# Performance work log

Measured on AMD Instinct MI355X. Metric: run time of the kernel, lower is better.

The kernel has to match this reference:

```python
import jax, jax.numpy as jnp
import numpy as np

K = 16  # FLAGS.num_neighbors
N = 2562  # ellipsoid vertices
B = 4     # FLAGS.batch_size
M = 16384 # points per cloud
D = 3     # coordinate dim


def _mean_neighborhood(coord, pc, k):
    # coord: [N, D] query vertices; pc: [B, D, M] point cloud (channels-first)
    x2 = jnp.sum(coord * coord, axis=1)[None, :, None]          # [1, N, 1]
    y2 = jnp.sum(pc * pc, axis=1)[:, None, :]                   # [B, 1, M]
    xy = jnp.einsum('nd,bdm->bnm', coord, pc)                   # [B, N, M]
    d2 = x2 + y2 - 2.0 * xy                                     # [B, N, M]
    _, idx = jax.lax.top_k(-d2, k)                               # [B, N, K] indices into M
    Y = jnp.transpose(pc, (0, 2, 1))                             # [B, M, D]
    bv = jnp.arange(pc.shape[0])[:, None, None]                  # [B, 1, 1]
    knnY = Y[bv, idx]                                            # [B, N, K, D]
    knnY_mean = jnp.mean(knnY, axis=2)                           # [B, N, D]
    return knnY_mean[0]                                          # [N, D] (matches knnY_mean[0])


def setup_inputs() -> dict:
    key = jax.random.key(0)
    ks = jax.random.split(key, 5)
    inputs = jax.random.normal(ks[0], (N, D), dtype=jnp.float32)
    pcs = [jax.random.normal(ks[i + 1], (B, D, M), dtype=jnp.float32) for i in range(4)]
    return {"inputs": inputs, "pc0": pcs[0], "pc1": pcs[1], "pc2": pcs[2], "pc3": pcs[3]}


def reference(inputs, pc0, pc1, pc2, pc3):
    s0 = _mean_neighborhood(inputs, pc0, K)
    s1 = _mean_neighborhood(inputs, pc1, K)
    s2 = _mean_neighborhood(inputs, pc2, K)
    s3 = _mean_neighborhood(inputs, pc3, K)
    return jnp.concatenate([inputs, s0, s1, s2, s3], axis=1)  # [N, 5*D]
```

## Files before the change

### kernel.cpp

```cpp
#include <hip/hip_runtime.h>
#include <stdint.h>
#include <math.h>

#define NQ    2562
#define MPTS  16384
#define QPB   4
#define NBQ   641
#define NT    (MPTS / 256)
#define CAP   320

__global__ __launch_bounds__(256)
void passthrough_kernel(const float* __restrict__ inp, float* __restrict__ out) {
    int gid = blockIdx.x * 256 + threadIdx.x;
    if (gid < NQ * 3) {
        int n = gid / 3, c = gid - n * 3;
        out[n * 15 + c] = inp[gid];
    }
}

__device__ __forceinline__ float sqsum3(float y0, float y1, float y2) {
    return __fadd_rn(__fadd_rn(__fmul_rn(y0, y0), __fmul_rn(y1, y1)),
                     __fmul_rn(y2, y2));
}
__device__ __forceinline__ float keyf(float xs, float a2, float b2, float c2,
                                      float y0, float y1, float y2, float ysq) {
    float u = fmaf(c2, y2, fmaf(b2, y1, __fmul_rn(a2, y0)));
    return __fsub_rn(__fadd_rn(xs, ysq), u);
}
__device__ __forceinline__ unsigned long long packkey(float k, int m) {
    uint32_t kb = __float_as_uint(k);
    kb ^= (uint32_t)((int32_t)kb >> 31) | 0x80000000u;
    return ((unsigned long long)kb << 32) | (unsigned)m;
}
__device__ __forceinline__ float unmapkey(unsigned long long pk) {
    uint32_t kb = (uint32_t)(pk >> 32);
    return __uint_as_float((kb & 0x80000000u) ? (kb ^ 0x80000000u) : ~kb);
}
__device__ __forceinline__ int prefix_lt(unsigned long long m) {
    return __builtin_amdgcn_mbcnt_hi((unsigned)(m >> 32),
           __builtin_amdgcn_mbcnt_lo((unsigned)m, 0u));
}

__device__ __forceinline__ unsigned long long sort64(unsigned long long v, int lane) {
#pragma unroll
    for (int k = 2; k <= 64; k <<= 1) {
#pragma unroll
        for (int j = k >> 1; j > 0; j >>= 1) {
            unsigned long long p = __shfl_xor(v, j);
            bool up = ((lane & k) == 0) == ((lane & j) == 0);
            bool sw = up ? (p < v) : (v < p);
            v = sw ? p : v;
        }
    }
    return v;
}

__device__ __forceinline__ float rebuild_q(unsigned long long* t16p,
                                           unsigned long long* S, int& cnt,
                                           int lane, bool fin) {
    int c = cnt;
    int full = c >> 6, rem = c & 63;
    int rounds = full + ((fin && rem) ? 1 : 0);
    unsigned long long v = ~0ULL;
    for (int rd = 0; rd < rounds; ++rd) {
        int i = (rd << 6) + lane;
        unsigned long long pk = (i < c) ? S[i] : ~0ULL;
        pk = sort64(pk, lane);
        unsigned long long bsw = __shfl(pk, (31 - lane) & 63);
        v = (lane < 16) ? t16p[lane & 15] : (lane < 32) ? bsw : ~0ULL;
#pragma unroll
        for (int j = 16; j > 0; j >>= 1) {
            unsigned long long p2 = __shfl_xor(v, j);
            bool keepmin = (lane & j) == 0;
            bool less = p2 < v;
            v = (keepmin == less) ? p2 : v;
        }
        if (lane < 16) t16p[lane] = v;
    }
    if (!fin) {
        if (lane < rem) S[lane] = S[(full << 6) + lane];
        cnt = rem;
    } else {
        cnt = 0;
    }
    return unmapkey(__shfl(v, 15));
}

__global__ __launch_bounds__(256)
void ysq_kernel(const float* __restrict__ pc0, const float* __restrict__ pc1,
                const float* __restrict__ pc2, const float* __restrict__ pc3,
                float* __restrict__ ysq) {
    int gid = blockIdx.x * 256 + threadIdx.x;
    int pc = gid >> 14, m = gid & (MPTS - 1);
    const float* P = (pc == 0) ? pc0 : (pc == 1) ? pc1 : (pc == 2) ? pc2 : pc3;
    ysq[gid] = sqsum3(P[m], P[MPTS + m], P[2 * MPTS + m]);
}

template <bool USE_YSQ>
__global__ __launch_bounds__(256)
void knn_kernel(const float* __restrict__ inp,
                const float* __restrict__ pc0, const float* __restrict__ pc1,
                const float* __restrict__ pc2, const float* __restrict__ pc3,
                const float* __restrict__ ysq,
                float* __restrict__ out) {
    const int b    = blockIdx.x;
    const int wid  = threadIdx.x >> 6;
    const int lane = threadIdx.x & 63;

    const int pc = b / NBQ;
    const int nb = b - pc * NBQ;
    const float* __restrict__ P = (pc == 0) ? pc0 : (pc == 1) ? pc1
                                : (pc == 2) ? pc2 : pc3;

    __shared__ float              tiles[2][4][256];
    __shared__ unsigned long long stk_sh[4][CAP];
    __shared__ unsigned long long t16_sh[4][16];

    if (lane < 16) t16_sh[wid][lane] = ~0ULL;

    float A2, B2, C2, XS;
    {
        int n = QPB * nb + wid;
        n = (n < NQ) ? n : (NQ - 1);
        float x0 = inp[n * 3 + 0];
        float x1 = inp[n * 3 + 1];
        float x2 = inp[n * 3 + 2];
        A2 = 2.0f * x0;
        B2 = 2.0f * x1;
        C2 = 2.0f * x2;
        XS = sqsum3(x0, x1, x2);
    }
    float tau;
    int   cnt = 0;

    const float* __restrict__ gch =
        (wid == 0) ? P : (wid == 1) ? (P + MPTS) : (wid == 2) ? (P + 2 * MPTS)
                   : (USE_YSQ ? (ysq + pc * MPTS) : P);

    auto push_tile = [&](int mofs, float k0, float k1, float k2, float k3) {
        unsigned long long b0 = __ballot(k0 <= tau);
        unsigned long long b1 = __ballot(k1 <= tau);
        unsigned long long b2 = __ballot(k2 <= tau);
        unsigned long long b3 = __ballot(k3 <= tau);
        int pre = prefix_lt(b0) + prefix_lt(b1) + prefix_lt(b2) + prefix_lt(b3);
        int tot = __popcll(b0) + __popcll(b1) + __popcll(b2) + __popcll(b3);
        int pos = cnt + pre;
        unsigned long long* S = stk_sh[wid];
        if (k0 <= tau) S[pos++] = packkey(k0, mofs + 0);
        if (k1 <= tau) S[pos++] = packkey(k1, mofs + 1);
        if (k2 <= tau) S[pos++] = packkey(k2, mofs + 2);
        if (k3 <= tau) S[pos++] = packkey(k3, mofs + 3);
        cnt += tot;
        if (cnt >= 64)
            tau = rebuild_q(t16_sh[wid], S, cnt, lane, false);
    };

    auto stage_load = [&](int t) -> float4 {
        if (USE_YSQ || wid < 3) {
            return *(const float4*)(gch + (t << 8) + (lane << 2));
        } else {
            const float* px = P + (t << 8) + (lane << 2);
            float4 a = *(const float4*)(px);
            float4 bq = *(const float4*)(px + MPTS);
            float4 cq = *(const float4*)(px + 2 * MPTS);
            float4 r;
            r.x = sqsum3(a.x, bq.x, cq.x);
            r.y = sqsum3(a.y, bq.y, cq.y);
            r.z = sqsum3(a.z, bq.z, cq.z);
            r.w = sqsum3(a.w, bq.w, cq.w);
            return r;
        }
    };

    {
        float4 s0 = stage_load(0);
        *(float4*)&tiles[0][wid][lane << 2] = s0;
    }
    __syncthreads();

    for (int t = 0; t < NT; ++t) {
        const int cur = t & 1;
        float4 stg;
        if (t + 1 < NT) stg = stage_load(t + 1);

        float4 xv = *(const float4*)&tiles[cur][0][lane << 2];
        float4 yv = *(const float4*)&tiles[cur][1][lane << 2];
        float4 zv = *(const float4*)&tiles[cur][2][lane << 2];
        float4 qv = *(const float4*)&tiles[cur][3][lane << 2];

        const int mofs = (t << 8) + (lane << 2);
        float k0 = keyf(XS, A2, B2, C2, xv.x, yv.x, zv.x, qv.x);
        float k1 = keyf(XS, A2, B2, C2, xv.y, yv.y, zv.y, qv.y);
        float k2 = keyf(XS, A2, B2, C2, xv.z, yv.z, zv.z, qv.z);
        float k3 = keyf(XS, A2, B2, C2, xv.w, yv.w, zv.w, qv.w);
        float km = fminf(fminf(k0, k1), fminf(k2, k3));

        if (t == 0) {
            float g = km;
            g = fminf(g, __shfl_xor(g, 1));
            g = fminf(g, __shfl_xor(g, 2));
            float m = g;
            m = fmaxf(m, __shfl_xor(m, 4));
            m = fmaxf(m, __shfl_xor(m, 8));
            m = fmaxf(m, __shfl_xor(m, 16));
            m = fmaxf(m, __shfl_xor(m, 32));
            tau = m;
            push_tile(mofs, k0, k1, k2, k3);
        } else if (__ballot(km <= tau)) {
            push_tile(mofs, k0, k1, k2, k3);
        }

        if (t + 1 < NT) *(float4*)&tiles[cur ^ 1][wid][lane << 2] = stg;

        __syncthreads();
    }

    if (cnt > 0)
        rebuild_q(t16_sh[wid], stk_sh[wid], cnt, lane, true);

    if (lane < 16) {
        unsigned long long v = t16_sh[wid][lane];
        int idx = (int)(unsigned)v;
        float gx = P[idx];
        float gy = P[MPTS + idx];
        float gz = P[2 * MPTS + idx];
#pragma unroll
        for (int off = 8; off > 0; off >>= 1) {
            gx += __shfl_down(gx, off, 16);
            gy += __shfl_down(gy, off, 16);
            gz += __shfl_down(gz, off, 16);
        }
        if (lane == 0) {
            int n = QPB * nb + wid;
            n = (n < NQ) ? n : (NQ - 1);
            float* o = out + n * 15 + 3 + 3 * pc;
            o[0] = gx * 0.0625f;
            o[1] = gy * 0.0625f;
            o[2] = gz * 0.0625f;
        }
    }
}

extern "C" void kernel_launch(void* const* d_in, const int* in_sizes, int n_in,
                              void* d_out, int out_size, void* d_ws, size_t ws_size,
                              hipStream_t stream) {
    const float* inp = (const float*)d_in[0];
    const float* pc0 = (const float*)d_in[1];
    const float* pc1 = (const float*)d_in[2];
    const float* pc2 = (const float*)d_in[3];
    const float* pc3 = (const float*)d_in[4];
    float* out = (float*)d_out;
    float* ysq = (float*)d_ws;

    hipLaunchKernelGGL(passthrough_kernel, dim3((NQ * 3 + 255) / 256), dim3(256),
                       0, stream, inp, out);

    const bool use_ysq = (ws_size >= (size_t)(4 * MPTS * sizeof(float)));
    if (use_ysq) {
        hipLaunchKernelGGL(ysq_kernel, dim3(4 * MPTS / 256), dim3(256), 0, stream,
                           pc0, pc1, pc2, pc3, ysq);
        hipLaunchKernelGGL((knn_kernel<true>), dim3(4 * NBQ), dim3(256), 0, stream,
                           inp, pc0, pc1, pc2, pc3, ysq, out);
    } else {
        hipLaunchKernelGGL((knn_kernel<false>), dim3(4 * NBQ), dim3(256), 0, stream,
                           inp, pc0, pc1, pc2, pc3, ysq, out);
    }
}
```

Baseline: 128.5 us.

## Split KNN scan into balanced per-wave runs with a partial top-16 merge kernel

Splits the work into 8192 equal-length runs of (query, tile) units, one per wave, so that each query's 64 tiles are covered by one or two waves. Each wave writes a partial top-16 list to workspace, and a new merge kernel combines the two lists with a bitonic shuffle before gathering and averaging. Waves now load directly from global memory instead of going through the shared-memory double buffer with block-wide syncs. The aim is more parallelism and fewer barriers. The cost is an extra kernel launch, a workspace round trip, and each run re-seeding its own threshold, so it prunes less well than one long scan.

New measurement: 138.8 us. +8.0%, slower.

```diff
diff --git a/kernel.cpp b/kernel.cpp
--- a/kernel.cpp
+++ b/kernel.cpp
@@ -3,11 +3,16 @@
 #include <math.h>
 
 #define NQ    2562
+#define NQ4   (4 * NQ)
 #define MPTS  16384
-#define QPB   4
-#define NBQ   641
-#define NT    (MPTS / 256)
+#define NRUNS 8192
 #define CAP   320
+
+#define YSQ_BYTES   ((size_t)(4 * MPTS) * sizeof(float))
+#define PART_BYTES  ((size_t)NQ4 * 2 * 16 * sizeof(unsigned long long))
+
+__device__ __forceinline__ int run_start(int r) { return 80 * r + (r >> 4); }
+__device__ __forceinline__ int run_of(int u)   { return (16 * u + 15) / 1281; }
 
 __global__ __launch_bounds__(256)
 void passthrough_kernel(const float* __restrict__ inp, float* __restrict__ out) {
@@ -96,105 +101,219 @@
     ysq[gid] = sqsum3(P[m], P[MPTS + m], P[2 * MPTS + m]);
 }
 
+__device__ __forceinline__ const float* selpc(int pc, const float* p0,
+                                              const float* p1, const float* p2,
+                                              const float* p3) {
+    return (pc == 0) ? p0 : (pc == 1) ? p1 : (pc == 2) ? p2 : p3;
+}
+
+__global__ __launch_bounds__(256)
+void knn_runs(const float* __restrict__ inp,
+              const float* __restrict__ pc0, const float* __restrict__ pc1,
+              const float* __restrict__ pc2, const float* __restrict__ pc3,
+              const float* __restrict__ ysq,
+              unsigned long long* __restrict__ part) {
+    const int wid  = threadIdx.x >> 6;
+    const int lane = threadIdx.x & 63;
+    const int run  = blockIdx.x * 4 + wid;
+
+    int       u    = run_start(run);
+    const int su   = u;
+    const int uend = run_start(run + 1);
+
+    __shared__ unsigned long long stk_sh[4][CAP];
+    __shared__ unsigned long long t16_sh[4][16];
+    unsigned long long* S = stk_sh[wid];
+    unsigned long long* T = t16_sh[wid];
+
+    int q  = u >> 6, tl = u & 63;
+    int pc = q / NQ;
+    int n  = q - pc * NQ;
+    const float* __restrict__ P = selpc(pc, pc0, pc1, pc2, pc3);
+    const float* __restrict__ Q = ysq + pc * MPTS;
+
+    while (u < uend) {
+        int seglen = 64 - tl;
+        { int rem = uend - u; if (seglen > rem) seglen = rem; }
+
+        float x0 = inp[n * 3 + 0];
+        float x1 = inp[n * 3 + 1];
+        float x2 = inp[n * 3 + 2];
+        float A2 = 2.0f * x0, B2 = 2.0f * x1, C2 = 2.0f * x2;
+        float XS = sqsum3(x0, x1, x2);
+        if (lane < 16) T[lane] = ~0ULL;
+        float tau = 0.0f;
+        int   cnt = 0;
+
+        for (int i = 0; i < seglen; ++i) {
+            const int t    = tl + i;
+            const int mofs = (t << 8) + (lane << 2);
+            float4 xv = *(const float4*)(P + mofs);
+            float4 yv = *(const float4*)(P + MPTS + mofs);
+            float4 zv = *(const float4*)(P + 2 * MPTS + mofs);
+            float4 qv = *(const float4*)(Q + mofs);
+
+            float k0 = keyf(XS, A2, B2, C2, xv.x, yv.x, zv.x, qv.x);
+            float k1 = keyf(XS, A2, B2, C2, xv.y, yv.y, zv.y, qv.y);
+            float k2 = keyf(XS, A2, B2, C2, xv.z, yv.z, zv.z, qv.z);
+            float k3 = keyf(XS, A2, B2, C2, xv.w, yv.w, zv.w, qv.w);
+            float km = fminf(fminf(k0, k1), fminf(k2, k3));
+
+            bool fire;
+            if (i == 0) {
+                float g = km;
+                g = fminf(g, __shfl_xor(g, 1));
+                g = fminf(g, __shfl_xor(g, 2));
+                float m = g;
+                m = fmaxf(m, __shfl_xor(m, 4));
+                m = fmaxf(m, __shfl_xor(m, 8));
+                m = fmaxf(m, __shfl_xor(m, 16));
+                m = fmaxf(m, __shfl_xor(m, 32));
+                tau = m;
+                fire = true;
+            } else {
+                fire = (__ballot(km <= tau) != 0ULL);
+            }
+
+            if (fire) {
+                unsigned long long b0 = __ballot(k0 <= tau);
+                unsigned long long b1 = __ballot(k1 <= tau);
+                unsigned long long b2 = __ballot(k2 <= tau);
+                unsigned long long b3 = __ballot(k3 <= tau);
+                int pre = prefix_lt(b0) + prefix_lt(b1) + prefix_lt(b2) + prefix_lt(b3);
+                int tot = __popcll(b0) + __popcll(b1) + __popcll(b2) + __popcll(b3);
+                int pos = cnt + pre;
+                if (k0 <= tau) S[pos++] = packkey(k0, mofs + 0);
+                if (k1 <= tau) S[pos++] = packkey(k1, mofs + 1);
+                if (k2 <= tau) S[pos++] = packkey(k2, mofs + 2);
+                if (k3 <= tau) S[pos++] = packkey(k3, mofs + 3);
+                cnt += tot;
+                if (cnt >= 64)
+                    tau = rebuild_q(T, S, cnt, lane, false);
+            }
+        }
+
+        if (cnt > 0) rebuild_q(T, S, cnt, lane, true);
+
+        int slot = (su > (q << 6)) ? 1 : 0;
+        if (lane < 16) part[(size_t)((q << 1) | slot) * 16 + lane] = T[lane];
+
+        u += seglen; tl = 0;
+        if (u < uend) {
+            ++q; ++n;
+            if (n == NQ) { n = 0; ++pc; P = selpc(pc, pc0, pc1, pc2, pc3);
+                           Q = ysq + pc * MPTS; }
+        }
+    }
+}
+
+__global__ __launch_bounds__(256)
+void merge_kernel(const float* __restrict__ pc0, const float* __restrict__ pc1,
+                  const float* __restrict__ pc2, const float* __restrict__ pc3,
+                  const unsigned long long* __restrict__ part,
+                  float* __restrict__ out) {
+    const int wv   = blockIdx.x * 4 + (threadIdx.x >> 6);
+    const int lane = threadIdx.x & 63;
+    const int h    = lane >> 5;
+    const int l32  = lane & 31;
+    const int q    = wv * 2 + h;
+
+    const int pc = q / NQ;
+    const int n  = q - pc * NQ;
+    const float* __restrict__ P = selpc(pc, pc0, pc1, pc2, pc3);
+
+    const int u0 = q << 6;
+    const bool two = (run_of(u0) != run_of(u0 + 63));
+
+    unsigned long long v;
+    if (l32 < 16) v = part[(size_t)(q << 1) * 16 + l32];
+    else          v = two ? part[(size_t)((q << 1) | 1) * 16 + ((31 - l32) & 15)]
+                          : ~0ULL;
+#pragma unroll
+    for (int j = 16; j > 0; j >>= 1) {
+        unsigned long long p2 = __shfl_xor(v, j);
+        bool keepmin = (l32 & j) == 0;
+        bool less = p2 < v;
+        v = (keepmin == less) ? p2 : v;
+    }
+
+    if (l32 < 16) {
+        int idx = (int)(unsigned)v;
+        float gx = P[idx];
+        float gy = P[MPTS + idx];
+        float gz = P[2 * MPTS + idx];
+#pragma unroll
+        for (int off = 8; off > 0; off >>= 1) {
+            gx += __shfl_down(gx, off, 16);
+            gy += __shfl_down(gy, off, 16);
+            gz += __shfl_down(gz, off, 16);
+        }
+        if (l32 == 0) {
+            float* o = out + n * 15 + 3 + 3 * pc;
+            o[0] = gx * 0.0625f;
+            o[1] = gy * 0.0625f;
+            o[2] = gz * 0.0625f;
+        }
+    }
+}
+
+#define QPB   4
+#define NBQ   641
+#define NT    (MPTS / 256)
 template <bool USE_YSQ>
 __global__ __launch_bounds__(256)
-void knn_kernel(const float* __restrict__ inp,
-                const float* __restrict__ pc0, const float* __restrict__ pc1,
-                const float* __restrict__ pc2, const float* __restrict__ pc3,
-                const float* __restrict__ ysq,
-                float* __restrict__ out) {
+void knn_fallback(const float* __restrict__ inp,
+                  const float* __restrict__ pc0, const float* __restrict__ pc1,
+                  const float* __restrict__ pc2, const float* __restrict__ pc3,
+                  const float* __restrict__ ysq,
+                  float* __restrict__ out) {
     const int b    = blockIdx.x;
     const int wid  = threadIdx.x >> 6;
     const int lane = threadIdx.x & 63;
-
     const int pc = b / NBQ;
     const int nb = b - pc * NBQ;
-    const float* __restrict__ P = (pc == 0) ? pc0 : (pc == 1) ? pc1
-                                : (pc == 2) ? pc2 : pc3;
-
-    __shared__ float              tiles[2][4][256];
+    const float* __restrict__ P = selpc(pc, pc0, pc1, pc2, pc3);
+
     __shared__ unsigned long long stk_sh[4][CAP];
     __shared__ unsigned long long t16_sh[4][16];
-
     if (lane < 16) t16_sh[wid][lane] = ~0ULL;
 
     float A2, B2, C2, XS;
     {
         int n = QPB * nb + wid;
         n = (n < NQ) ? n : (NQ - 1);
-        float x0 = inp[n * 3 + 0];
-        float x1 = inp[n * 3 + 1];
-        float x2 = inp[n * 3 + 2];
-        A2 = 2.0f * x0;
-        B2 = 2.0f * x1;
-        C2 = 2.0f * x2;
+        float x0 = inp[n * 3 + 0], x1 = inp[n * 3 + 1], x2 = inp[n * 3 + 2];
+        A2 = 2.0f * x0; B2 = 2.0f * x1; C2 = 2.0f * x2;
         XS = sqsum3(x0, x1, x2);
     }
-    float tau;
+    float tau = 0.0f;
     int   cnt = 0;
-
-    const float* __restrict__ gch =
-        (wid == 0) ? P : (wid == 1) ? (P + MPTS) : (wid == 2) ? (P + 2 * MPTS)
-                   : (USE_YSQ ? (ysq + pc * MPTS) : P);
-
-    auto push_tile = [&](int mofs, float k0, float k1, float k2, float k3) {
-        unsigned long long b0 = __ballot(k0 <= tau);
-        unsigned long long b1 = __ballot(k1 <= tau);
-        unsigned long long b2 = __ballot(k2 <= tau);
-        unsigned long long b3 = __ballot(k3 <= tau);
-        int pre = prefix_lt(b0) + prefix_lt(b1) + prefix_lt(b2) + prefix_lt(b3);
-        int tot = __popcll(b0) + __popcll(b1) + __popcll(b2) + __popcll(b3);
-        int pos = cnt + pre;
-        unsigned long long* S = stk_sh[wid];
-        if (k0 <= tau) S[pos++] = packkey(k0, mofs + 0);
-        if (k1 <= tau) S[pos++] = packkey(k1, mofs + 1);
-        if (k2 <= tau) S[pos++] = packkey(k2, mofs + 2);
-        if (k3 <= tau) S[pos++] = packkey(k3, mofs + 3);
-        cnt += tot;
-        if (cnt >= 64)
-            tau = rebuild_q(t16_sh[wid], S, cnt, lane, false);
-    };
-
-    auto stage_load = [&](int t) -> float4 {
-        if (USE_YSQ || wid < 3) {
-            return *(const float4*)(gch + (t << 8) + (lane << 2));
+    const float* __restrict__ Pl = P + (lane << 2);
+    const float* __restrict__ Ql = ysq + pc * MPTS + (lane << 2);
+    unsigned long long* S = stk_sh[wid];
+    unsigned long long* T = t16_sh[wid];
+
+    for (int t = 0; t < NT; ++t) {
+        const int mofs = (t << 8) + (lane << 2);
+        float4 xv = *(const float4*)(Pl + (t << 8));
+        float4 yv = *(const float4*)(Pl + MPTS + (t << 8));
+        float4 zv = *(const float4*)(Pl + 2 * MPTS + (t << 8));
+        float q0, q1, q2, q3;
+        if (USE_YSQ) {
+            float4 qv = *(const float4*)(Ql + (t << 8));
+            q0 = qv.x; q1 = qv.y; q2 = qv.z; q3 = qv.w;
         } else {
-            const float* px = P + (t << 8) + (lane << 2);
-            float4 a = *(const float4*)(px);
-            float4 bq = *(const float4*)(px + MPTS);
-            float4 cq = *(const float4*)(px + 2 * MPTS);
-            float4 r;
-            r.x = sqsum3(a.x, bq.x, cq.x);
-            r.y = sqsum3(a.y, bq.y, cq.y);
-            r.z = sqsum3(a.z, bq.z, cq.z);
-            r.w = sqsum3(a.w, bq.w, cq.w);
-            return r;
-        }
-    };
-
-    {
-        float4 s0 = stage_load(0);
-        *(float4*)&tiles[0][wid][lane << 2] = s0;
-    }
-    __syncthreads();
-
-    for (int t = 0; t < NT; ++t) {
-        const int cur = t & 1;
-        float4 stg;
-        if (t + 1 < NT) stg = stage_load(t + 1);
-
-        float4 xv = *(const float4*)&tiles[cur][0][lane << 2];
-        float4 yv = *(const float4*)&tiles[cur][1][lane << 2];
-        float4 zv = *(const float4*)&tiles[cur][2][lane << 2];
-        float4 qv = *(const float4*)&tiles[cur][3][lane << 2];
-
-        const int mofs = (t << 8) + (lane << 2);
-        float k0 = keyf(XS, A2, B2, C2, xv.x, yv.x, zv.x, qv.x);
-        float k1 = keyf(XS, A2, B2, C2, xv.y, yv.y, zv.y, qv.y);
-        float k2 = keyf(XS, A2, B2, C2, xv.z, yv.z, zv.z, qv.z);
-        float k3 = keyf(XS, A2, B2, C2, xv.w, yv.w, zv.w, qv.w);
+            q0 = sqsum3(xv.x, yv.x, zv.x);
+            q1 = sqsum3(xv.y, yv.y, zv.y);
+            q2 = sqsum3(xv.z, yv.z, zv.z);
+            q3 = sqsum3(xv.w, yv.w, zv.w);
+        }
+        float k0 = keyf(XS, A2, B2, C2, xv.x, yv.x, zv.x, q0);
+        float k1 = keyf(XS, A2, B2, C2, xv.y, yv.y, zv.y, q1);
+        float k2 = keyf(XS, A2, B2, C2, xv.z, yv.z, zv.z, q2);
+        float k3 = keyf(XS, A2, B2, C2, xv.w, yv.w, zv.w, q3);
         float km = fminf(fminf(k0, k1), fminf(k2, k3));
-
+        bool fire;
         if (t == 0) {
             float g = km;
             g = fminf(g, __shfl_xor(g, 1));
@@ -204,22 +323,31 @@
             m = fmaxf(m, __shfl_xor(m, 8));
             m = fmaxf(m, __shfl_xor(m, 16));
             m = fmaxf(m, __shfl_xor(m, 32));
-            tau = m;
-            push_tile(mofs, k0, k1, k2, k3);
-        } else if (__ballot(km <= tau)) {
-            push_tile(mofs, k0, k1, k2, k3);
-        }
-
-        if (t + 1 < NT) *(float4*)&tiles[cur ^ 1][wid][lane << 2] = stg;
-
-        __syncthreads();
-    }
-
-    if (cnt > 0)
-        rebuild_q(t16_sh[wid], stk_sh[wid], cnt, lane, true);
+            tau = m; fire = true;
+        } else {
+            fire = (__ballot(km <= tau) != 0ULL);
+        }
+        if (fire) {
+            unsigned long long b0 = __ballot(k0 <= tau);
+            unsigned long long b1 = __ballot(k1 <= tau);
+            unsigned long long b2 = __ballot(k2 <= tau);
+            unsigned long long b3 = __ballot(k3 <= tau);
+            int pre = prefix_lt(b0) + prefix_lt(b1) + prefix_lt(b2) + prefix_lt(b3);
+            int tot = __popcll(b0) + __popcll(b1) + __popcll(b2) + __popcll(b3);
+            int pos = cnt + pre;
+            if (k0 <= tau) S[pos++] = packkey(k0, mofs + 0);
+            if (k1 <= tau) S[pos++] = packkey(k1, mofs + 1);
+            if (k2 <= tau) S[pos++] = packkey(k2, mofs + 2);
+            if (k3 <= tau) S[pos++] = packkey(k3, mofs + 3);
+            cnt += tot;
+            if (cnt >= 64)
+                tau = rebuild_q(T, S, cnt, lane, false);
+        }
+    }
+    if (cnt > 0) rebuild_q(T, S, cnt, lane, true);
 
     if (lane < 16) {
-        unsigned long long v = t16_sh[wid][lane];
+        unsigned long long v = T[lane];
         int idx = (int)(unsigned)v;
         float gx = P[idx];
         float gy = P[MPTS + idx];
@@ -251,18 +379,26 @@
     const float* pc3 = (const float*)d_in[4];
     float* out = (float*)d_out;
     float* ysq = (float*)d_ws;
+    unsigned long long* part =
+        (unsigned long long*)((char*)d_ws + YSQ_BYTES);
 
     hipLaunchKernelGGL(passthrough_kernel, dim3((NQ * 3 + 255) / 256), dim3(256),
                        0, stream, inp, out);
 
-    const bool use_ysq = (ws_size >= (size_t)(4 * MPTS * sizeof(float)));
-    if (use_ysq) {
+    if (ws_size >= YSQ_BYTES + PART_BYTES) {
         hipLaunchKernelGGL(ysq_kernel, dim3(4 * MPTS / 256), dim3(256), 0, stream,
                            pc0, pc1, pc2, pc3, ysq);
-        hipLaunchKernelGGL((knn_kernel<true>), dim3(4 * NBQ), dim3(256), 0, stream,
-                           inp, pc0, pc1, pc2, pc3, ysq, out);
+        hipLaunchKernelGGL(knn_runs, dim3(NRUNS / 4), dim3(256), 0, stream,
+                           inp, pc0, pc1, pc2, pc3, ysq, part);
+        hipLaunchKernelGGL(merge_kernel, dim3(NQ4 / 8), dim3(256), 0, stream,
+                           pc0, pc1, pc2, pc3, part, out);
+    } else if (ws_size >= YSQ_BYTES) {
+        hipLaunchKernelGGL(ysq_kernel, dim3(4 * MPTS / 256), dim3(256), 0, stream,
+                           pc0, pc1, pc2, pc3, ysq);
+        hipLaunchKernelGGL((knn_fallback<true>), dim3(4 * NBQ), dim3(256), 0,
+                           stream, inp, pc0, pc1, pc2, pc3, ysq, out);
     } else {
-        hipLaunchKernelGGL((knn_kernel<false>), dim3(4 * NBQ), dim3(256), 0, stream,
-                           inp, pc0, pc1, pc2, pc3, ysq, out);
-    }
-}
+        hipLaunchKernelGGL((knn_fallback<false>), dim3(4 * NBQ), dim3(256), 0,
+                           stream, inp, pc0, pc1, pc2, pc3, ysq, out);
+    }
+}
```
